# Kernel optimization log

Measured on AMD Instinct MI355X. Metric: run time of the kernel, lower is better.

## Reference

```python
import jax, jax.numpy as jnp
import numpy as np

# Dimensions matching init_kwargs
B, T, F = 256, 512, 128
COH_PTS, BULK_PTS, OUT_LEN = 64, 128, 6
COH_SIZE = 2 * COH_PTS            # fc11 out
IN_BULK = F + COH_PTS             # fc12 in
BULK_SIZE = 3 * BULK_PTS          # fc12 out

# Material constants (Turon cohesive bilinear law + J2 plasticity w/ linear hardening)
DELTA0, DELTAF = 0.01, 0.1        # damage onset / final equivalent jump
E_MOD, NU = 1.0e3, 0.3
G_MOD = E_MOD / (2.0 * (1.0 + NU))
SIG_Y, HARD = 10.0, 100.0
EPS = 1e-12
LEAKY_SLOPE = 0.01


def _plane_stress_D():
    c = E_MOD / (1.0 - NU * NU)
    return jnp.array([[c, c * NU, 0.0],
                      [c * NU, c, 0.0],
                      [0.0, 0.0, c * (1.0 - NU) / 2.0]], dtype=jnp.float32)


def setup_inputs() -> dict:
    key = jax.random.key(0)
    k_x, k_w11, k_b11, k_w12, k_w2 = jax.random.split(key, 5)
    scale11 = 1.0 / np.sqrt(F)
    scale12 = 1.0 / np.sqrt(IN_BULK)
    scale2 = 1.0 / np.sqrt(BULK_SIZE)
    return {
        "x": jax.random.normal(k_x, (B, T, F), dtype=jnp.float32),
        "W11": jax.random.normal(k_w11, (COH_SIZE, F), dtype=jnp.float32) * scale11,
        "b11": jax.random.normal(k_b11, (COH_SIZE,), dtype=jnp.float32) * scale11,
        "W12": jax.random.normal(k_w12, (BULK_SIZE, IN_BULK), dtype=jnp.float32) * scale12,
        "W2": jax.random.normal(k_w2, (OUT_LEN, BULK_SIZE), dtype=jnp.float32) * scale2,
    }


def reference(x, W11, b11, W12, W2):
    b, t, f = x.shape
    coh_pts = W11.shape[0] // 2
    bulk_pts = W12.shape[0] // 3
    D = _plane_stress_D()

    # fc11 (leaky-relu linear) is history-free -> vectorize over all timesteps
    jumps = jax.nn.leaky_relu(jnp.einsum('btf,cf->btc', x, W11) + b11,
                              LEAKY_SLOPE).reshape(b, t, coh_pts, 2)

    def step(carry, inp):
        dmg, ep = carry                      # [b, coh_pts], [b, bulk_pts]
        x_t, jump_t = inp                    # [b, f], [b, coh_pts, 2]

        # --- Turon cohesive update: monotone bilinear damage on equivalent jump ---
        jn = jax.nn.relu(jump_t[..., 0])     # tension-only normal jump
        js = jump_t[..., 1]
        delta = jnp.sqrt(jn * jn + js * js + EPS)
        d_new = jnp.clip(DELTAF * (delta - DELTA0)
                         / (jnp.maximum(delta, EPS) * (DELTAF - DELTA0)), 0.0, 1.0)
        dmg = jnp.maximum(dmg, d_new)        # commit: damage never heals

        # --- midini = cat(input, damages) -> fc12 (no bias) ---
        midini = jnp.concatenate([x_t, dmg], axis=-1)          # [b, f+coh_pts]
        strain = (midini @ W12.T).reshape(b, bulk_pts, 3)       # [b, bulk_pts, 3]

        # --- J2 plasticity (plane stress, radial return, linear hardening) ---
        sig_tr = jnp.einsum('bpi,ji->bpj', strain, D)           # trial stress
        sxx, syy, txy = sig_tr[..., 0], sig_tr[..., 1], sig_tr[..., 2]
        seq = jnp.sqrt(sxx * sxx - sxx * syy + syy * syy + 3.0 * txy * txy + EPS)
        fyield = seq - (SIG_Y + HARD * ep)
        dep = jnp.where(fyield > 0.0, fyield / (3.0 * G_MOD + HARD), 0.0)
        ep = ep + dep                                           # commit history
        scale = jnp.where(fyield > 0.0, (SIG_Y + HARD * ep) / seq, 1.0)
        sig = sig_tr * scale[..., None]

        # --- fc2 (softLayer: linear no bias + softplus) ---
        out_t = jax.nn.softplus(sig.reshape(b, -1) @ W2.T)      # [b, out_len]
        return (dmg, ep), out_t

    carry0 = (jnp.zeros((b, coh_pts), jnp.float32),
              jnp.zeros((b, bulk_pts), jnp.float32))
    _, out = jax.lax.scan(step, carry0,
                          (jnp.swapaxes(x, 0, 1), jnp.swapaxes(jumps, 0, 1)))
    return jnp.swapaxes(out, 0, 1)           # [b, t, out_len]
```

## Files before the change

kernel.cpp:

```cpp
#include <hip/hip_runtime.h>
#include <hip/hip_bf16.h>
#include <math.h>

#define NB 256
#define NT 512
#define NF 128
#define NCOH 64
#define NIN 192
#define NBS 384
#define NROWS (NB*NT)

#define C11 1098.9010989010989f
#define C12 329.67032967032966f
#define C33 384.61538461538464f
#define H3G 1253.8461538461538f
#define HOVER 0.07975460122699386f

typedef __attribute__((ext_vector_type(8))) short bf16x8;
typedef __attribute__((ext_vector_type(4))) float f32x4;
typedef __attribute__((ext_vector_type(8))) unsigned short ushort8v;
typedef __attribute__((ext_vector_type(4))) unsigned short ushort4v;

#define WAITCNT_VM(N) __builtin_amdgcn_s_waitcnt(0x0F70 | ((N) & 15) | (((N) >> 4) << 14))

#define PS ((size_t)NROWS * 32)
__device__ unsigned short g_Ahi[6 * PS];
__device__ unsigned short g_Alo[4 * PS];
__device__ unsigned short g_Bres[2 * NBS * NIN];
__device__ unsigned short g_W11res[32768];

static __device__ __forceinline__ unsigned short f2bf(float v) {
    __hip_bfloat16 h = __float2bfloat16(v);
    return *reinterpret_cast<unsigned short*>(&h);
}
static __device__ __forceinline__ float bf2f(unsigned short u) {
    unsigned int x = ((unsigned int)u) << 16;
    return *reinterpret_cast<float*>(&x);
}
static __device__ __forceinline__ void async_copy16(const void* g, void* l) {
    __builtin_amdgcn_global_load_lds(
        (const __attribute__((address_space(1))) unsigned int*)g,
        (__attribute__((address_space(3))) unsigned int*)l, 16, 0, 0);
}

__global__ __launch_bounds__(256) void k0_w12(const float* __restrict__ W12)
{
    const int idx = blockIdx.x * 256 + threadIdx.x;
    const int e    = idx & 7;
    const int l    = (idx >> 3) & 63;
    const int nf   = (idx >> 9) & 3;
    const int part = (idx >> 11) & 1;
    const int kc   = (idx >> 12) % 6;
    const int nblk = idx / 24576;
    const int n = nblk * 64 + nf * 16 + (l & 15);
    const int k = kc * 32 + (l >> 4) * 8 + e;
    const int p = n / 3, j = n - 3 * p;
    const float* w = W12 + (size_t)(3 * p) * NIN;
    float v;
    if (j == 0)      v = C11 * w[k]           + C12 * w[NIN + k];
    else if (j == 1) v = C12 * w[k]           + C11 * w[NIN + k];
    else             v = C33 * w[2 * NIN + k];
    unsigned short h = f2bf(v);
    g_Bres[idx] = part ? f2bf(v - bf2f(h)) : h;
}

__global__ __launch_bounds__(256) void k0b_w11(const float* __restrict__ W11)
{
    const int idx = blockIdx.x * 256 + threadIdx.x;
    const int e    = idx & 7;
    const int l    = (idx >> 3) & 63;
    const int nf   = (idx >> 9) & 7;
    const int part = (idx >> 12) & 1;
    const int kc   = idx >> 13;
    const int n = nf * 16 + (l & 15);
    const int k = kc * 32 + (l >> 4) * 8 + e;
    const float v = W11[(size_t)n * NF + k];
    unsigned short h = f2bf(v);
    g_W11res[idx] = part ? f2bf(v - bf2f(h)) : h;
}

__global__ __launch_bounds__(256) void kx_split(const float* __restrict__ x)
{
    const int idx = blockIdx.x * 256 + threadIdx.x;
    const int row = idx >> 4, g = idx & 15;
    const float* src = x + (size_t)row * NF + g * 8;
    float4 v0 = ((const float4*)src)[0];
    float4 v1 = ((const float4*)src)[1];
    float v[8] = {v0.x, v0.y, v0.z, v0.w, v1.x, v1.y, v1.z, v1.w};
    ushort8v h, lo;
#pragma unroll
    for (int i = 0; i < 8; ++i) {
        h[i]  = f2bf(v[i]);
        lo[i] = f2bf(v[i] - bf2f(h[i]));
    }
    const size_t off = (size_t)(g >> 2) * PS + (size_t)row * 32 + (g & 3) * 8;
    *(ushort8v*)(g_Ahi + off) = h;
    *(ushort8v*)(g_Alo + off) = lo;
}

__global__ __launch_bounds__(256) void k1_fc11(
    const float* __restrict__ b11, unsigned short* __restrict__ dnT)
{
    __shared__ unsigned short Ws[32768];

    const int tid = threadIdx.x;
    const int lane = tid & 63, w = tid >> 6;
    const int fr = lane & 15, fq = lane >> 4;
    const int xbase = blockIdx.x * 128 + w * 32;

#pragma unroll
    for (int i = 0; i < 16; ++i)
        async_copy16((const char*)g_W11res + tid * 16 + i * 4096,
                     (char*)Ws + tid * 16 + i * 4096);

    f32x4 acc[8][2];
#pragma unroll
    for (int q = 0; q < 8; ++q)
#pragma unroll
        for (int f = 0; f < 2; ++f) acc[q][f] = (f32x4){0.f, 0.f, 0.f, 0.f};

    WAITCNT_VM(0);
    __builtin_amdgcn_s_barrier();

#pragma unroll
    for (int kc = 0; kc < 4; ++kc) {
        bf16x8 ah[2], al[2];
#pragma unroll
        for (int f = 0; f < 2; ++f) {
            const size_t off = (size_t)kc * PS
                             + (size_t)(xbase + f * 16 + fr) * 32 + fq * 8;
            ah[f] = *(const bf16x8*)(g_Ahi + off);
            al[f] = *(const bf16x8*)(g_Alo + off);
        }
#pragma unroll
        for (int q = 0; q < 8; ++q) {
            bf16x8 wh = *(const bf16x8*)&Ws[(kc * 16 + q) * 512 + lane * 8];
            bf16x8 wl = *(const bf16x8*)&Ws[(kc * 16 + 8 + q) * 512 + lane * 8];
#pragma unroll
            for (int f = 0; f < 2; ++f) {
                acc[q][f] = __builtin_amdgcn_mfma_f32_16x16x32_bf16(
                    wh, ah[f], acc[q][f], 0, 0, 0);
                acc[q][f] = __builtin_amdgcn_mfma_f32_16x16x32_bf16(
                    wl, ah[f], acc[q][f], 0, 0, 0);
                acc[q][f] = __builtin_amdgcn_mfma_f32_16x16x32_bf16(
                    wh, al[f], acc[q][f], 0, 0, 0);
            }
        }
    }

#pragma unroll
    for (int q = 0; q < 8; ++q) {
        float4 bv = *(const float4*)(b11 + q * 16 + fq * 4);
#pragma unroll
        for (int f = 0; f < 2; ++f) {
            const int xrow = xbase + f * 16 + fr;
            float z[4] = {acc[q][f][0] + bv.x, acc[q][f][1] + bv.y,
                          acc[q][f][2] + bv.z, acc[q][f][3] + bv.w};
#pragma unroll
            for (int pr = 0; pr < 2; ++pr) {
                float jn = fmaxf(z[2 * pr], 0.0f);
                float zs = z[2 * pr + 1];
                float js = (zs > 0.0f) ? zs : 0.01f * zs;
                float delta = sqrtf(jn * jn + js * js + 1e-12f);
                float dn = 0.1f * (delta - 0.01f) / (fmaxf(delta, 1e-12f) * 0.09f);
                dn = fminf(fmaxf(dn, 0.0f), 1.0f);
                dnT[(size_t)(q * 8 + fq * 2 + pr) * NROWS + xrow] = f2bf(dn);
            }
        }
    }
}

__global__ __launch_bounds__(64) void k2a(const unsigned short* __restrict__ dnT,
                                          float* __restrict__ totals)
{
    const int b = blockIdx.x >> 3, seg = blockIdx.x & 7;
    const int c = threadIdx.x;
    const ushort8v* p = (const ushort8v*)(dnT + (size_t)c * NROWS + b * NT + seg * 64);
    float m = 0.0f;
#pragma unroll
    for (int g = 0; g < 8; ++g) {
        ushort8v v = p[g];
#pragma unroll
        for (int i = 0; i < 8; ++i) m = fmaxf(m, bf2f(v[i]));
    }
    totals[(size_t)(b * 8 + seg) * 64 + c] = m;
}

__global__ __launch_bounds__(64) void k2b(const unsigned short* __restrict__ dnT,
                                          const float* __restrict__ totals)
{
    const int b = blockIdx.x >> 3, seg = blockIdx.x & 7;
    const int c = threadIdx.x;
    float carry = 0.0f;
    for (int s = 0; s < seg; ++s)
        carry = fmaxf(carry, totals[(size_t)(b * 8 + s) * 64 + c]);
    const ushort8v* p = (const ushort8v*)(dnT + (size_t)c * NROWS + b * NT + seg * 64);
    unsigned short* ah = g_Ahi + (size_t)(4 + (c >> 5)) * PS
                       + (size_t)(b * NT + seg * 64) * 32 + (c & 31);
    float m = carry;
#pragma unroll
    for (int g = 0; g < 8; ++g) {
        ushort8v v = p[g];
#pragma unroll
        for (int i = 0; i < 8; ++i) {
            m = fmaxf(m, bf2f(v[i]));
            ah[(size_t)(g * 8 + i) * 32] = f2bf(m);
        }
    }
}

__global__ __launch_bounds__(256, 3) void k3_mfma(unsigned short* __restrict__ sigT)
{
    __shared__ unsigned short Bs[24576];

    const int tid = threadIdx.x;
    const int lane = tid & 63, w = tid >> 6;
    const int id = blockIdx.x;
    const int sw = (id & 7) * 384 + (id >> 3);
    const int nblk = sw % 6;
    const int m0 = (sw / 6) * 256;
    const int n0 = nblk * 64;
    const int wm = w * 64;
    const int fr = lane & 15, fq = lane >> 4;

    const size_t abase = (size_t)(m0 + wm + fr) * 32 + fq * 8;

    bf16x8 a0[4], a1[4];
#pragma unroll
    for (int mi = 0; mi < 4; ++mi)
        a0[mi] = *(const bf16x8*)(g_Ahi + abase + mi * 512);

    {
        const char* bsrc = (const char*)g_Bres + (size_t)nblk * 49152;
#pragma unroll
        for (int i = 0; i < 12; ++i)
            async_copy16(bsrc + tid * 16 + i * 4096, (char*)Bs + tid * 16 + i * 4096);
    }
    WAITCNT_VM(0);
    __builtin_amdgcn_s_barrier();

    f32x4 acc[4][4];
#pragma unroll
    for (int mi = 0; mi < 4; ++mi)
#pragma unroll
        for (int ni = 0; ni < 4; ++ni) acc[mi][ni] = (f32x4){0.f, 0.f, 0.f, 0.f};

#pragma unroll
    for (int c = 0; c < 6; ++c) {
        bf16x8* acur = (c & 1) ? a1 : a0;
        bf16x8* anxt = (c & 1) ? a0 : a1;
        if (c < 5) {
#pragma unroll
            for (int mi = 0; mi < 4; ++mi)
                anxt[mi] = *(const bf16x8*)(g_Ahi + (size_t)(c + 1) * PS
                                            + abase + mi * 512);
        }
        bf16x8 bh[4], bl[4];
#pragma unroll
        for (int ni = 0; ni < 4; ++ni) {
            bh[ni] = *(const bf16x8*)&Bs[((c * 8 + ni) << 9) + lane * 8];
            bl[ni] = *(const bf16x8*)&Bs[((c * 8 + 4 + ni) << 9) + lane * 8];
        }
#pragma unroll
        for (int mi = 0; mi < 4; ++mi)
#pragma unroll
            for (int ni = 0; ni < 4; ++ni) {
                acc[mi][ni] = __builtin_amdgcn_mfma_f32_16x16x32_bf16(
                    acur[mi], bh[ni], acc[mi][ni], 0, 0, 0);
                acc[mi][ni] = __builtin_amdgcn_mfma_f32_16x16x32_bf16(
                    acur[mi], bl[ni], acc[mi][ni], 0, 0, 0);
            }
    }

    const int b_idx = m0 >> 9;
    const int tbase = (m0 & 511) + wm + fq * 4;
#pragma unroll
    for (int mi = 0; mi < 4; ++mi)
#pragma unroll
        for (int ni = 0; ni < 4; ++ni) {
            const int col = n0 + ni * 16 + fr;
            ushort4v h;
#pragma unroll
            for (int r = 0; r < 4; ++r) h[r] = f2bf(acc[mi][ni][r]);
            *(ushort4v*)(sigT + (((size_t)(b_idx * NBS + col)) << 9)
                              + tbase + mi * 16) = h;
        }
}

#define PFD 8
__global__ __launch_bounds__(128) void k4_scan(
    const unsigned short* __restrict__ sigT, unsigned short* __restrict__ uT)
{
    const int b = blockIdx.x;
    const int p = threadIdx.x;
    const ushort8v* sx = (const ushort8v*)(sigT + (((size_t)(b * NBS + 3 * p    )) << 9));
    const ushort8v* sy = (const ushort8v*)(sigT + (((size_t)(b * NBS + 3 * p + 1)) << 9));
    const ushort8v* sz = (const ushort8v*)(sigT + (((size_t)(b * NBS + 3 * p + 2)) << 9));
    ushort8v* uo = (ushort8v*)(uT + (((size_t)(b * 128 + p)) << 9));

    ushort8v px[PFD], py[PFD], pz[PFD];
#pragma unroll
    for (int g = 0; g < PFD; ++g) { px[g] = sx[g]; py[g] = sy[g]; pz[g] = sz[g]; }

    float u = 10.0f;
#pragma unroll 8
    for (int g = 0; g < 64 - PFD; ++g) {
        const int sl = g & (PFD - 1);
        ushort8v vx = px[sl], vy = py[sl], vz = pz[sl];
        px[sl] = sx[g + PFD]; py[sl] = sy[g + PFD]; pz[sl] = sz[g + PFD];
        ushort8v ov;
#pragma unroll
        for (int i = 0; i < 8; ++i) {
            float sxx = bf2f(vx[i]), syy = bf2f(vy[i]), txy = bf2f(vz[i]);
            float e = sxx*sxx - sxx*syy + syy*syy + 3.0f*txy*txy + 1e-12f;
            float seq = sqrtf(e);
            u = fmaf(fmaxf(seq - u, 0.0f), HOVER, u);
            ov[i] = f2bf(u);
        }
        uo[g] = ov;
    }
#pragma unroll
    for (int g = 64 - PFD; g < 64; ++g) {
        const int sl = g & (PFD - 1);
        ushort8v vx = px[sl], vy = py[sl], vz = pz[sl];
        ushort8v ov;
#pragma unroll
        for (int i = 0; i < 8; ++i) {
            float sxx = bf2f(vx[i]), syy = bf2f(vy[i]), txy = bf2f(vz[i]);
            float e = sxx*sxx - sxx*syy + syy*syy + 3.0f*txy*txy + 1e-12f;
            float seq = sqrtf(e);
            u = fmaf(fmaxf(seq - u, 0.0f), HOVER, u);
            ov[i] = f2bf(u);
        }
        uo[g] = ov;
    }
}

__global__ __launch_bounds__(256) void k5_out(
    const unsigned short* __restrict__ sigT, const unsigned short* __restrict__ uT,
    const float* __restrict__ W2, float* __restrict__ out)
{
    __shared__ float W2s[6][NBS];
    const int tid = threadIdx.x;
    for (int i = tid; i < 6 * NBS; i += 256) W2s[i / NBS][i % NBS] = W2[i];
    __syncthreads();

    const int b = blockIdx.x >> 1;
    const int t = (blockIdx.x & 1) * 256 + tid;
    const unsigned short* sb = sigT + (((size_t)b * NBS) << 9) + t;
    const unsigned short* ub = uT + (((size_t)b * 128) << 9) + t;

    float acc[6] = {0, 0, 0, 0, 0, 0};
#pragma unroll 4
    for (int p = 0; p < 128; ++p) {
        float sxx = bf2f(sb[(size_t)(3 * p    ) << 9]);
        float syy = bf2f(sb[(size_t)(3 * p + 1) << 9]);
        float txy = bf2f(sb[(size_t)(3 * p + 2) << 9]);
        float u   = bf2f(ub[(size_t)p << 9]);
        float e = sxx*sxx - sxx*syy + syy*syy + 3.0f*txy*txy + 1e-12f;
        float scale = fminf(1.0f, u * rsqrtf(e));
        float fx = sxx * scale, fy = syy * scale, fz = txy * scale;
#pragma unroll
        for (int o = 0; o < 6; ++o) {
            acc[o] = fmaf(fx, W2s[o][3 * p    ], acc[o]);
            acc[o] = fmaf(fy, W2s[o][3 * p + 1], acc[o]);
            acc[o] = fmaf(fz, W2s[o][3 * p + 2], acc[o]);
        }
    }

    float* op = out + ((size_t)(b * NT + t)) * 6;
#pragma unroll
    for (int o = 0; o < 6; ++o) {
        float z = acc[o];
        op[o] = fmaxf(z, 0.0f) + log1pf(expf(-fabsf(z)));
    }
}

extern "C" void kernel_launch(void* const* d_in, const int* in_sizes, int n_in,
                              void* d_out, int out_size, void* d_ws, size_t ws_size,
                              hipStream_t stream)
{
    const float* x   = (const float*)d_in[0];
    const float* W11 = (const float*)d_in[1];
    const float* b11 = (const float*)d_in[2];
    const float* W12 = (const float*)d_in[3];
    const float* W2  = (const float*)d_in[4];
    float* out = (float*)d_out;

    unsigned short* dnT = (unsigned short*)d_ws;
    unsigned short* uT = (unsigned short*)d_ws;
    unsigned short* sigT = (unsigned short*)((char*)d_ws + (size_t)NROWS * NCOH * sizeof(float));
    float* totals = (float*)((char*)d_ws + (size_t)128 * 1024 * 1024);

    k0_w12<<<(2 * NBS * NIN) / 256, 256, 0, stream>>>(W12);
    k0b_w11<<<128, 256, 0, stream>>>(W11);
    kx_split<<<(NROWS * 16) / 256, 256, 0, stream>>>(x);
    k1_fc11<<<NROWS / 128, 256, 0, stream>>>(b11, dnT);
    k2a<<<NB * 8, 64, 0, stream>>>(dnT, totals);
    k2b<<<NB * 8, 64, 0, stream>>>(dnT, totals);
    k3_mfma<<<3072, 256, 0, stream>>>(sigT);
    k4_scan<<<NB, 128, 0, stream>>>(sigT, uT);
    k5_out<<<NROWS / 256, 256, 0, stream>>>(sigT, uT, W2, out);
}
```

Measured before the change: 295.3 us.

## Make k3 MFMA blocks loop over four M tiles with triple-buffered A prefetch

Each k3 block now handles four 256-row M tiles in sequence, so the grid shrinks from 3072 to 768 blocks. The 48KB B tile is loaded into LDS once and reused four times instead of being reloaded by every block. A loads move to a three-deep register ring that prefetches two chunks ahead, crossing tile boundaries, and s_setprio raises wave priority around the MFMA bursts. The trade-off is fewer blocks to spread across CUs, higher register pressure from the extra A buffer, and epilogue stores that now sit inside the loop.

Result: slower. 412.2 us (+39.6%).

```diff
diff --git a/kernel.cpp b/kernel.cpp
--- a/kernel.cpp
+++ b/kernel.cpp
@@ -216,26 +216,30 @@
     const int tid = threadIdx.x;
     const int lane = tid & 63, w = tid >> 6;
     const int id = blockIdx.x;
-    const int sw = (id & 7) * 384 + (id >> 3);
+    const int sw = (id & 7) * 96 + (id >> 3);
     const int nblk = sw % 6;
-    const int m0 = (sw / 6) * 256;
+    const int mgrp = sw / 6;
     const int n0 = nblk * 64;
     const int wm = w * 64;
     const int fr = lane & 15, fq = lane >> 4;
 
-    const size_t abase = (size_t)(m0 + wm + fr) * 32 + fq * 8;
-
-    bf16x8 a0[4], a1[4];
-#pragma unroll
-    for (int mi = 0; mi < 4; ++mi)
-        a0[mi] = *(const bf16x8*)(g_Ahi + abase + mi * 512);
-
     {
         const char* bsrc = (const char*)g_Bres + (size_t)nblk * 49152;
 #pragma unroll
         for (int i = 0; i < 12; ++i)
             async_copy16(bsrc + tid * 16 + i * 4096, (char*)Bs + tid * 16 + i * 4096);
     }
+
+    const size_t abase0 = (size_t)(mgrp * 1024 + wm + fr) * 32 + fq * 8;
+
+    bf16x8 abuf[3][4];
+#pragma unroll
+    for (int mi = 0; mi < 4; ++mi)
+        abuf[0][mi] = *(const bf16x8*)(g_Ahi + abase0 + mi * 512);
+#pragma unroll
+    for (int mi = 0; mi < 4; ++mi)
+        abuf[1][mi] = *(const bf16x8*)(g_Ahi + PS + abase0 + mi * 512);
+
     WAITCNT_VM(0);
     __builtin_amdgcn_s_barrier();
 
@@ -245,46 +249,56 @@
 #pragma unroll
         for (int ni = 0; ni < 4; ++ni) acc[mi][ni] = (f32x4){0.f, 0.f, 0.f, 0.f};
 
-#pragma unroll
-    for (int c = 0; c < 6; ++c) {
-        bf16x8* acur = (c & 1) ? a1 : a0;
-        bf16x8* anxt = (c & 1) ? a0 : a1;
-        if (c < 5) {
+#pragma unroll 1
+    for (int t = 0; t < 4; ++t) {
+        const size_t ab_t = abase0 + (size_t)t * 8192;
+#pragma unroll
+        for (int c = 0; c < 6; ++c) {
+            {
+                const int pc = c + 2;
+                const int pk = (pc < 6) ? pc : pc - 6;
+                const size_t pb = (pc < 6) ? ab_t : ab_t + 8192;
+                if ((pc < 6) || (t < 3)) {
+#pragma unroll
+                    for (int mi = 0; mi < 4; ++mi)
+                        abuf[pc % 3][mi] = *(const bf16x8*)(
+                            g_Ahi + (size_t)pk * PS + pb + mi * 512);
+                }
+            }
+            bf16x8 bh[4], bl[4];
+#pragma unroll
+            for (int ni = 0; ni < 4; ++ni) {
+                bh[ni] = *(const bf16x8*)&Bs[((c * 8 + ni) << 9) + lane * 8];
+                bl[ni] = *(const bf16x8*)&Bs[((c * 8 + 4 + ni) << 9) + lane * 8];
+            }
+            __builtin_amdgcn_s_setprio(1);
 #pragma unroll
             for (int mi = 0; mi < 4; ++mi)
-                anxt[mi] = *(const bf16x8*)(g_Ahi + (size_t)(c + 1) * PS
-                                            + abase + mi * 512);
-        }
-        bf16x8 bh[4], bl[4];
-#pragma unroll
-        for (int ni = 0; ni < 4; ++ni) {
-            bh[ni] = *(const bf16x8*)&Bs[((c * 8 + ni) << 9) + lane * 8];
-            bl[ni] = *(const bf16x8*)&Bs[((c * 8 + 4 + ni) << 9) + lane * 8];
-        }
+#pragma unroll
+                for (int ni = 0; ni < 4; ++ni) {
+                    acc[mi][ni] = __builtin_amdgcn_mfma_f32_16x16x32_bf16(
+                        abuf[c % 3][mi], bh[ni], acc[mi][ni], 0, 0, 0);
+                    acc[mi][ni] = __builtin_amdgcn_mfma_f32_16x16x32_bf16(
+                        abuf[c % 3][mi], bl[ni], acc[mi][ni], 0, 0, 0);
+                }
+            __builtin_amdgcn_s_setprio(0);
+        }
+
+        const int b_idx = mgrp * 2 + (t >> 1);
+        const int tbase = (t & 1) * 256 + wm + fq * 4;
 #pragma unroll
         for (int mi = 0; mi < 4; ++mi)
 #pragma unroll
             for (int ni = 0; ni < 4; ++ni) {
-                acc[mi][ni] = __builtin_amdgcn_mfma_f32_16x16x32_bf16(
-                    acur[mi], bh[ni], acc[mi][ni], 0, 0, 0);
-                acc[mi][ni] = __builtin_amdgcn_mfma_f32_16x16x32_bf16(
-                    acur[mi], bl[ni], acc[mi][ni], 0, 0, 0);
+                const int col = n0 + ni * 16 + fr;
+                ushort4v h;
+#pragma unroll
+                for (int r = 0; r < 4; ++r) h[r] = f2bf(acc[mi][ni][r]);
+                *(ushort4v*)(sigT + (((size_t)(b_idx * NBS + col)) << 9)
+                                  + tbase + mi * 16) = h;
+                acc[mi][ni] = (f32x4){0.f, 0.f, 0.f, 0.f};
             }
     }
-
-    const int b_idx = m0 >> 9;
-    const int tbase = (m0 & 511) + wm + fq * 4;
-#pragma unroll
-    for (int mi = 0; mi < 4; ++mi)
-#pragma unroll
-        for (int ni = 0; ni < 4; ++ni) {
-            const int col = n0 + ni * 16 + fr;
-            ushort4v h;
-#pragma unroll
-            for (int r = 0; r < 4; ++r) h[r] = f2bf(acc[mi][ni][r]);
-            *(ushort4v*)(sigT + (((size_t)(b_idx * NBS + col)) << 9)
-                              + tbase + mi * 16) = h;
-        }
 }
 
 #define PFD 8
@@ -398,7 +412,7 @@
     k1_fc11<<<NROWS / 128, 256, 0, stream>>>(b11, dnT);
     k2a<<<NB * 8, 64, 0, stream>>>(dnT, totals);
     k2b<<<NB * 8, 64, 0, stream>>>(dnT, totals);
-    k3_mfma<<<3072, 256, 0, stream>>>(sigT);
+    k3_mfma<<<768, 256, 0, stream>>>(sigT);
     k4_scan<<<NB, 128, 0, stream>>>(sigT, uT);
     k5_out<<<NROWS / 256, 256, 0, stream>>>(sigT, uT, W2, out);
 }
```
